# Performance work log

Hardware: AMD Instinct MI355X
Metric: run time of the kernel (lower is better)

Reference implementation:

```python
import jax, jax.numpy as jnp
import numpy as np

N = 64      # features
L = 96      # history length
LP = 24     # prediction length
H = 128     # rnn hidden
B = 1024    # batch


def setup_inputs() -> dict:
    key = jax.random.key(0)
    ks = jax.random.split(key, 16)
    # monotonically increasing timestamps
    tp_all = jnp.cumsum(jax.random.uniform(ks[0], (B, L + LP), dtype=jnp.float32), axis=1)
    tp_true = tp_all[:, :L]
    tp_pred = tp_all[:, L:]
    X = jax.random.normal(ks[1], (B, L, N), dtype=jnp.float32)
    mask = jax.random.randint(ks[2], (B, L, N), 0, 2).astype(jnp.float32)
    def unif(k, shape, fan):
        std = 1.0 / np.sqrt(fan)
        return jax.random.uniform(k, shape, jnp.float32, -std, std)
    # TemporalDecay for h: W (H,N), b (H); std = 1/sqrt(out)
    Wh_dec = unif(ks[3], (H, N), H)
    bh_dec = unif(ks[4], (H,), H)
    # TemporalDecay for x (diag): W (N,N) but only diagonal used
    Wx_dec = unif(ks[5], (N, N), N)
    bx_dec = unif(ks[6], (N,), N)
    # GRUCell: input size = 2N + H
    in_sz = 2 * N + H
    W_ih = unif(ks[7], (3 * H, in_sz), H)
    W_hh = unif(ks[8], (3 * H, H), H)
    b_ih = unif(ks[9], (3 * H,), H)
    b_hh = unif(ks[10], (3 * H,), H)
    # output projection
    Wp = unif(ks[11], (N, H), H)
    bp = unif(ks[12], (N,), H)
    return {"tp_pred": tp_pred, "X": X, "tp_true": tp_true, "mask": mask,
            "Wh_dec": Wh_dec, "bh_dec": bh_dec, "Wx_dec": Wx_dec, "bx_dec": bx_dec,
            "W_ih": W_ih, "W_hh": W_hh, "b_ih": b_ih, "b_hh": b_hh,
            "Wp": Wp, "bp": bp}


def _grud(tp_pred, X, tp_true, mask, Wh_dec, bh_dec, Wx_dec, bx_dec,
          W_ih, W_hh, b_ih, b_hh, Wp, bp):
    Bsz, Lh, Nf = X.shape
    Lp = tp_pred.shape[1]
    Lall = Lh + Lp
    Hh = Wh_dec.shape[0]

    # pad future with zeros (unobserved)
    X_all = jnp.concatenate([X, jnp.zeros((Bsz, Lp, Nf), X.dtype)], axis=1)
    M_all = jnp.concatenate([mask, jnp.zeros((Bsz, Lp, Nf), X.dtype)], axis=1)
    tp = jnp.concatenate([tp_true, tp_pred], axis=1)

    # deltas: first-difference padded with 0 at t=0, broadcast over features
    dt = jnp.pad(tp[:, 1:] - tp[:, :-1], ((0, 0), (1, 0)))  # (B, Lall)
    deltas = jnp.broadcast_to(dt[:, :, None], (Bsz, Lall, Nf))

    # empirical mean over positions where (1 - mask) == 1 (faithful to source)
    valid = 1.0 - M_all
    cnt = jnp.clip(valid.sum(axis=1), 1.0, None)  # (B, N)
    mu = (X_all * valid).sum(axis=1) / cnt        # (B, N)

    # LOCF as in source: where mask != 0, copy previous value
    def locf_step(prev, xm):
        x_t, m_t = xm
        cur = jnp.where(m_t != 0, prev, x_t)
        return cur, cur
    _, X_locf = jax.lax.scan(locf_step, X_all[:, 0],
                             (jnp.swapaxes(X_all, 0, 1), jnp.swapaxes(M_all, 0, 1)))
    # X_locf: (Lall, B, N)

    diag_Wx = jnp.diag(Wx_dec)  # (N,) -- diag=True masks W with identity

    def step(h, inputs):
        x_t, m_t, d_t, xl_t = inputs  # each (B, N)
        gh = jnp.exp(-jax.nn.relu(d_t @ Wh_dec.T + bh_dec))      # (B, H)
        gx = jnp.exp(-jax.nn.relu(d_t * diag_Wx + bx_dec))       # (B, N)
        h = h * gh
        rep = h
        x_h = gx * xl_t + (1.0 - gx) * mu
        x_in = m_t * x_t + (1.0 - m_t) * x_h
        inp = jnp.concatenate([x_in, h, m_t], axis=1)             # (B, 2N+H)
        gi = inp @ W_ih.T + b_ih                                  # (B, 3H)
        gr = h @ W_hh.T + b_hh                                    # (B, 3H)
        r = jax.nn.sigmoid(gi[:, :Hh] + gr[:, :Hh])
        z = jax.nn.sigmoid(gi[:, Hh:2 * Hh] + gr[:, Hh:2 * Hh])
        n = jnp.tanh(gi[:, 2 * Hh:] + r * gr[:, 2 * Hh:])
        h_new = (1.0 - z) * n + z * h
        return h_new, rep

    h0 = jnp.zeros((Bsz, Hh), X.dtype)
    xs = (jnp.swapaxes(X_all, 0, 1), jnp.swapaxes(M_all, 0, 1),
          jnp.swapaxes(deltas, 0, 1), X_locf)
    _, reps = jax.lax.scan(step, h0, xs)          # (Lall, B, H)
    reps = jnp.swapaxes(reps, 0, 1)               # (B, Lall, H)
    recon = reps @ Wp.T + bp                      # (B, Lall, N)
    y_hat = recon[:, -Lp:]                        # (B, Lp, N)
    return y_hat[None]                            # (1, B, Lp, N)


def reference(tp_pred, X, tp_true, mask, Wh_dec, bh_dec, Wx_dec, bx_dec,
              W_ih, W_hh, b_ih, b_hh, Wp, bp):
    return _grud(tp_pred, X, tp_true, mask, Wh_dec, bh_dec, Wx_dec, bx_dec,
                 W_ih, W_hh, b_ih, b_hh, Wp, bp)
```

## Files before the change

kernel.cpp:

```cpp
#include <hip/hip_runtime.h>

#define L2E 1.4426950408889634f

typedef _Float16 f16x8 __attribute__((ext_vector_type(8)));
typedef _Float16 f16x4 __attribute__((ext_vector_type(4)));
typedef float f32x4 __attribute__((ext_vector_type(4)));

__device__ __forceinline__ float sig_fast(float x) {
    return __builtin_amdgcn_rcpf(1.0f + __builtin_amdgcn_exp2f(-L2E * x));
}
__device__ __forceinline__ float tanh_fast(float x) {
    return 1.0f - 2.0f * __builtin_amdgcn_rcpf(1.0f + __builtin_amdgcn_exp2f(2.0f * L2E * x));
}
__device__ __forceinline__ float expnr_fast(float x) {
    return __builtin_amdgcn_exp2f(-L2E * fmaxf(x, 0.0f));
}
__device__ __forceinline__ void barrier_lds_only() {
    __asm__ volatile("s_waitcnt lgkmcnt(0)\n\ts_barrier" ::: "memory");
}

struct F8 { float v[8]; };
__device__ __forceinline__ F8 ld8(const float* p) {
    F8 r;
    float4 a = *(const float4*)p, b = *(const float4*)(p + 4);
    r.v[0]=a.x; r.v[1]=a.y; r.v[2]=a.z; r.v[3]=a.w;
    r.v[4]=b.x; r.v[5]=b.y; r.v[6]=b.z; r.v[7]=b.w;
    return r;
}
__device__ __forceinline__ f16x8 cvt8(F8 a) {
    f16x8 r;
#pragma unroll
    for (int q = 0; q < 8; ++q) r[q] = (_Float16)a.v[q];
    return r;
}
__device__ __forceinline__ f16x8 cvt8s(F8 a, F8 b) {
    f16x8 r;
#pragma unroll
    for (int q = 0; q < 8; ++q) r[q] = (_Float16)(a.v[q] + b.v[q]);
    return r;
}

__global__ __launch_bounds__(256, 1) void grud_kernel(
    const float* __restrict__ tp_pred, const float* __restrict__ X,
    const float* __restrict__ tp_true, const float* __restrict__ mask,
    const float* __restrict__ Wh_dec, const float* __restrict__ bh_dec,
    const float* __restrict__ Wx_dec, const float* __restrict__ bx_dec,
    const float* __restrict__ W_ih, const float* __restrict__ W_hh,
    const float* __restrict__ b_ih, const float* __restrict__ b_hh,
    const float* __restrict__ Wp, const float* __restrict__ bp,
    float* __restrict__ out)
{
    constexpr int SR = 136;
    __shared__ alignas(16) _Float16 ring[16 * 1536];
    __shared__ alignas(16) _Float16 V[2][16 * SR];
    __shared__ alignas(16) _Float16 Astage[2][16 * SR];
    __shared__ float dt_lds[480];
    __shared__ float mu_l[4][64];
    __shared__ float wxl[64], bxl[64];
    __shared__ char occupancy_pad[32768];

    const int tid  = threadIdx.x;
    const int w    = tid >> 6, l = tid & 63, quad = l >> 4, lm = l & 15;
    const int b0   = blockIdx.x * 4;

    if (tid > 100000) occupancy_pad[0] = 1;

    for (int i = tid; i < 16 * SR; i += 256) ((unsigned*)V)[i] = 0;

    for (int i = tid; i < 480; i += 256) {
        int t = i >> 2, q = i & 3, b = b0 + q;
        float v = 0.0f;
        if (t) {
            float cur = (t < 96) ? tp_true[b * 96 + t] : tp_pred[b * 24 + t - 96];
            float prv = (t - 1 < 96) ? tp_true[b * 96 + t - 1] : tp_pred[b * 24 + t - 97];
            v = cur - prv;
        }
        dt_lds[i] = v;
    }
    if (tid < 64) { wxl[tid] = Wx_dec[tid * 65]; bxl[tid] = bx_dec[tid]; }

    {
        const float* xr = X    + ((size_t)(b0 + w) * 96) * 64 + l;
        const float* mr = mask + ((size_t)(b0 + w) * 96) * 64 + l;
        float a = 0.0f, c = 0.0f;
#pragma unroll 4
        for (int t = 0; t < 96; ++t) {
            float x = xr[t * 64], m = mr[t * 64];
            a += x * (1.0f - m); c += 1.0f - m;
        }
        mu_l[w][l] = a / (c + 24.0f);
    }

    const int c0 = 32 * w + lm, c1 = c0 + 16;

    f16x8 wxf[3][2][4];
#pragma unroll
    for (int g = 0; g < 3; ++g)
#pragma unroll
        for (int j = 0; j < 2; ++j)
#pragma unroll
            for (int fi = 0; fi < 4; ++fi) {
                const int row = g * 128 + (j ? c1 : c0);
                const int k0 = fi * 32 + quad * 8;
                wxf[g][j][fi] = cvt8(ld8(W_ih + row * 256 + (k0 < 64 ? k0 : 128 + k0)));
            }

    f16x8 wRZ[2][2][4], wNf[2][4], wGf[2][4], wPf[4];
    float S_[2], bh_[2], bR_[2], bZ_[2], bN_[2], bG_[2];
#pragma unroll
    for (int j = 0; j < 2; ++j) {
        const int c = j ? c1 : c0;
#pragma unroll
        for (int fi = 0; fi < 4; ++fi) {
            const int k0 = fi * 32 + quad * 8;
            wRZ[0][j][fi] = cvt8s(ld8(W_ih + c * 256 + 64 + k0),
                                  ld8(W_hh + c * 128 + k0));
            wRZ[1][j][fi] = cvt8s(ld8(W_ih + (128 + c) * 256 + 64 + k0),
                                  ld8(W_hh + (128 + c) * 128 + k0));
            wNf[j][fi] = cvt8(ld8(W_ih + (256 + c) * 256 + 64 + k0));
            wGf[j][fi] = cvt8(ld8(W_hh + (256 + c) * 128 + k0));
        }
        float s = 0.0f;
        const float4* wh4 = (const float4*)(Wh_dec + c * 64);
#pragma unroll
        for (int i = 0; i < 16; ++i) { float4 u = wh4[i]; s += u.x + u.y + u.z + u.w; }
        S_[j]  = s;
        bh_[j] = bh_dec[c];
        bR_[j] = b_ih[c] + b_hh[c];
        bZ_[j] = b_ih[128 + c] + b_hh[128 + c];
        bN_[j] = b_ih[256 + c];
        bG_[j] = b_hh[256 + c];
    }
    const int pn = w * 16 + lm;
    const float bpv = bp[pn];
#pragma unroll
    for (int fi = 0; fi < 4; ++fi)
        wPf[fi] = cvt8(ld8(Wp + pn * 128 + fi * 32 + quad * 8));

    auto prodLoad = [&](int gp, float4& px, float4& pm) {
        if (gp >= 24) { px = make_float4(0,0,0,0); pm = make_float4(0,0,0,0); return; }
        const int R = tid >> 4, tg = 4 * gp + (R >> 2), b = R & 3;
        const size_t o = (((size_t)(b0 + b) * 96) + tg) * 64 + (tid & 15) * 4;
        px = *(const float4*)(X + o);
        pm = *(const float4*)(mask + o);
    };
    auto prodStage = [&](int gp, float4 px, float4 pm) {
        const int R = tid >> 4, toff = R >> 2, b = R & 3;
        const int tg = 4 * gp + toff, n0 = (tid & 15) * 4;
        const float d = dt_lds[tg * 4 + b];
        const float xs[4] = {px.x, px.y, px.z, px.w};
        const float ms[4] = {pm.x, pm.y, pm.z, pm.w};
        f16x4 xi, mm;
#pragma unroll
        for (int e = 0; e < 4; ++e) {
            const int n = n0 + e;
            const float gxv = expnr_fast(d * wxl[n] + bxl[n]);
            const float muv = mu_l[b][n];
            float v;
            if (gp < 24) {
                v = (ms[e] != 0.0f) ? xs[e] : (xs[e] - muv) * gxv + muv;
                mm[e] = (_Float16)ms[e];
            } else {
                v = (1.0f - gxv) * muv;
                mm[e] = (_Float16)0.0f;
            }
            xi[e] = (_Float16)v;
        }
        *(f16x4*)&Astage[gp & 1][R * SR + n0]      = xi;
        *(f16x4*)&Astage[gp & 1][R * SR + 64 + n0] = mm;
    };
    auto prodMMA = [&](int gp, int j) {
        f16x8 ap[4];
#pragma unroll
        for (int fi = 0; fi < 4; ++fi)
            ap[fi] = *(const f16x8*)&Astage[gp & 1][lm * SR + fi * 32 + quad * 8];
        const int tg = 4 * gp + quad, slot = tg & 15;
        const int c = j ? c1 : c0;
#pragma unroll
        for (int g = 0; g < 3; ++g) {
            f32x4 acc = {0, 0, 0, 0};
#pragma unroll
            for (int fi = 0; fi < 4; ++fi)
                acc = __builtin_amdgcn_mfma_f32_16x16x32_f16(ap[fi], wxf[g][j][fi], acc, 0, 0, 0);
            f16x4 pk = {(_Float16)acc[0], (_Float16)acc[1], (_Float16)acc[2], (_Float16)acc[3]};
            *(f16x4*)&ring[slot * 1536 + (g * 128 + c) * 4] = pk;
        }
    };

    float h0 = 0.0f, h1 = 0.0f;

    auto step = [&](int t, auto&& extra) {
        const int p = t & 1;
        f16x8 af[4];
#pragma unroll
        for (int fi = 0; fi < 4; ++fi)
            af[fi] = *(const f16x8*)&V[p][lm * SR + fi * 32 + quad * 8];
        const int slot = t & 15;
        _Float16 g6[6];
#pragma unroll
        for (int j = 0; j < 2; ++j)
#pragma unroll
            for (int g = 0; g < 3; ++g)
                g6[j * 3 + g] = ring[slot * 1536 + (g * 128 + (j ? c1 : c0)) * 4 + quad];

        extra();

        f32x4 aR0 = {(float)g6[0] + bR_[0], 0, 0, 0}, aZ0 = {(float)g6[1] + bZ_[0], 0, 0, 0};
        f32x4 aN0 = {(float)g6[2] + bN_[0], 0, 0, 0}, aG0 = {bG_[0], 0, 0, 0};
        f32x4 aR1 = {(float)g6[3] + bR_[1], 0, 0, 0}, aZ1 = {(float)g6[4] + bZ_[1], 0, 0, 0};
        f32x4 aN1 = {(float)g6[5] + bN_[1], 0, 0, 0}, aG1 = {bG_[1], 0, 0, 0};
#pragma unroll
        for (int fi = 0; fi < 4; ++fi) {
            aR0 = __builtin_amdgcn_mfma_f32_16x16x32_f16(af[fi], wRZ[0][0][fi], aR0, 0, 0, 0);
            aZ0 = __builtin_amdgcn_mfma_f32_16x16x32_f16(af[fi], wRZ[1][0][fi], aZ0, 0, 0, 0);
            aN0 = __builtin_amdgcn_mfma_f32_16x16x32_f16(af[fi], wNf[0][fi], aN0, 0, 0, 0);
            aG0 = __builtin_amdgcn_mfma_f32_16x16x32_f16(af[fi], wGf[0][fi], aG0, 0, 0, 0);
            aR1 = __builtin_amdgcn_mfma_f32_16x16x32_f16(af[fi], wRZ[0][1][fi], aR1, 0, 0, 0);
            aZ1 = __builtin_amdgcn_mfma_f32_16x16x32_f16(af[fi], wRZ[1][1][fi], aZ1, 0, 0, 0);
            aN1 = __builtin_amdgcn_mfma_f32_16x16x32_f16(af[fi], wNf[1][fi], aN1, 0, 0, 0);
            aG1 = __builtin_amdgcn_mfma_f32_16x16x32_f16(af[fi], wGf[1][fi], aG1, 0, 0, 0);
        }
        if (t >= 96) {
            f32x4 aP = {bpv, 0, 0, 0};
#pragma unroll
            for (int fi = 0; fi < 4; ++fi)
                aP = __builtin_amdgcn_mfma_f32_16x16x32_f16(af[fi], wPf[fi], aP, 0, 0, 0);
            out[((size_t)(b0 + quad) * 24 + (t - 96)) * 64 + pn] = aP[0];
        }
        {
            const float rg0 = sig_fast(aR0[0]), zg0 = sig_fast(aZ0[0]);
            const float ng0 = tanh_fast(aN0[0] + rg0 * aG0[0]);
            h0 = zg0 * (h0 - ng0) + ng0;
            const float rg1 = sig_fast(aR1[0]), zg1 = sig_fast(aZ1[0]);
            const float ng1 = tanh_fast(aN1[0] + rg1 * aG1[0]);
            h1 = zg1 * (h1 - ng1) + ng1;
        }
        if (t < 119) {
            const float d = dt_lds[(t + 1) * 4 + quad];
            h0 *= expnr_fast(d * S_[0] + bh_[0]);
            h1 *= expnr_fast(d * S_[1] + bh_[1]);
            V[p ^ 1][(4 * quad) * SR + c0] = (_Float16)h0;
            V[p ^ 1][(4 * quad) * SR + c1] = (_Float16)h1;
        }
        barrier_lds_only();
    };

    {
        float4 px0, pm0, px1, pm1;
        prodLoad(0, px0, pm0);
        prodLoad(1, px1, pm1);
        __syncthreads();
        prodStage(0, px0, pm0);
        prodStage(1, px1, pm1);
        __syncthreads();
        prodMMA(0, 0); prodMMA(0, 1);
        prodMMA(1, 0); prodMMA(1, 1);
        barrier_lds_only();
    }

    for (int k = 0; k < 30; ++k) {
        const int gp = k + 2;
        float4 px, pm;
        step(4 * k + 0, [&] { if (gp < 30) prodLoad(gp, px, pm); });
        step(4 * k + 1, [&] { if (gp < 30) prodStage(gp, px, pm); });
        step(4 * k + 2, [&] { if (gp < 30) prodMMA(gp, 0); });
        step(4 * k + 3, [&] { if (gp < 30) prodMMA(gp, 1); });
    }
}

extern "C" void kernel_launch(void* const* d_in, const int* in_sizes, int n_in,
                              void* d_out, int out_size, void* d_ws, size_t ws_size,
                              hipStream_t stream) {
    const float* tp_pred = (const float*)d_in[0];
    const float* X       = (const float*)d_in[1];
    const float* tp_true = (const float*)d_in[2];
    const float* mask    = (const float*)d_in[3];
    const float* Wh_dec  = (const float*)d_in[4];
    const float* bh_dec  = (const float*)d_in[5];
    const float* Wx_dec  = (const float*)d_in[6];
    const float* bx_dec  = (const float*)d_in[7];
    const float* W_ih    = (const float*)d_in[8];
    const float* W_hh    = (const float*)d_in[9];
    const float* b_ih    = (const float*)d_in[10];
    const float* b_hh    = (const float*)d_in[11];
    const float* Wp      = (const float*)d_in[12];
    const float* bp      = (const float*)d_in[13];

    grud_kernel<<<dim3(256), dim3(256), 0, stream>>>(
        tp_pred, X, tp_true, mask, Wh_dec, bh_dec, Wx_dec, bx_dec,
        W_ih, W_hh, b_ih, b_hh, Wp, bp, (float*)d_out);
}
```

Before: 232.5 us.

## Split block into producer and recurrence wavefronts for GRU-D

Doubles the block to 512 threads. Four wavefronts do the input-side work (loading, imputation, input-projection MFMAs, output projection) and four run the hidden-state recurrence. The aim is to take producer work off the serial critical path of each timestep. The ring layout is repacked so one consumer lane reads its R/Z/N values with a single f16x4 load. The cost is twice the waves per block, a larger register budget split, and every step still needs a full-block barrier.

```diff
diff --git a/kernel.cpp b/kernel.cpp
--- a/kernel.cpp
+++ b/kernel.cpp
@@ -40,7 +40,7 @@
     return r;
 }
 
-__global__ __launch_bounds__(256, 1) void grud_kernel(
+__global__ __launch_bounds__(512, 2) void grud_kernel(
     const float* __restrict__ tp_pred, const float* __restrict__ X,
     const float* __restrict__ tp_true, const float* __restrict__ mask,
     const float* __restrict__ Wh_dec, const float* __restrict__ bh_dec,
@@ -51,220 +51,235 @@
     float* __restrict__ out)
 {
     constexpr int SR = 136;
-    __shared__ alignas(16) _Float16 ring[16 * 1536];
+    __shared__ alignas(16) _Float16 ring[8 * 2048];
     __shared__ alignas(16) _Float16 V[2][16 * SR];
-    __shared__ alignas(16) _Float16 Astage[2][16 * SR];
+    __shared__ alignas(16) _Float16 Astage[16 * SR];
     __shared__ float dt_lds[480];
     __shared__ float mu_l[4][64];
     __shared__ float wxl[64], bxl[64];
-    __shared__ char occupancy_pad[32768];
+    __shared__ char occ_pad[34000];
 
     const int tid  = threadIdx.x;
     const int w    = tid >> 6, l = tid & 63, quad = l >> 4, lm = l & 15;
     const int b0   = blockIdx.x * 4;
 
-    if (tid > 100000) occupancy_pad[0] = 1;
-
-    for (int i = tid; i < 16 * SR; i += 256) ((unsigned*)V)[i] = 0;
-
-    for (int i = tid; i < 480; i += 256) {
-        int t = i >> 2, q = i & 3, b = b0 + q;
+    if (tid > 100000) occ_pad[0] = 1;
+
+    for (int i = tid; i < 16 * SR; i += 512) ((unsigned*)V)[i] = 0;
+
+    if (tid < 480) {
+        int t = tid >> 2, q = tid & 3, b = b0 + q;
         float v = 0.0f;
         if (t) {
             float cur = (t < 96) ? tp_true[b * 96 + t] : tp_pred[b * 24 + t - 96];
             float prv = (t - 1 < 96) ? tp_true[b * 96 + t - 1] : tp_pred[b * 24 + t - 97];
             v = cur - prv;
         }
-        dt_lds[i] = v;
+        dt_lds[tid] = v;
     }
     if (tid < 64) { wxl[tid] = Wx_dec[tid * 65]; bxl[tid] = bx_dec[tid]; }
 
-    {
-        const float* xr = X    + ((size_t)(b0 + w) * 96) * 64 + l;
-        const float* mr = mask + ((size_t)(b0 + w) * 96) * 64 + l;
-        float a = 0.0f, c = 0.0f;
+    if (w >= 4) {
+        const int pw   = w - 4;
+        const int ptid = tid - 256;
+        const int c0   = 32 * pw + lm, c1 = c0 + 16;
+
+        {
+            const float* xr = X    + ((size_t)(b0 + pw) * 96) * 64 + l;
+            const float* mr = mask + ((size_t)(b0 + pw) * 96) * 64 + l;
+            float a = 0.0f, c = 0.0f;
 #pragma unroll 4
-        for (int t = 0; t < 96; ++t) {
-            float x = xr[t * 64], m = mr[t * 64];
-            a += x * (1.0f - m); c += 1.0f - m;
-        }
-        mu_l[w][l] = a / (c + 24.0f);
-    }
-
-    const int c0 = 32 * w + lm, c1 = c0 + 16;
-
-    f16x8 wxf[3][2][4];
-#pragma unroll
-    for (int g = 0; g < 3; ++g)
-#pragma unroll
-        for (int j = 0; j < 2; ++j)
+            for (int t = 0; t < 96; ++t) {
+                float x = xr[t * 64], m = mr[t * 64];
+                a += x * (1.0f - m); c += 1.0f - m;
+            }
+            mu_l[pw][l] = a / (c + 24.0f);
+        }
+
+        f16x8 wxf[3][2][4];
+#pragma unroll
+        for (int g = 0; g < 3; ++g)
+#pragma unroll
+            for (int j = 0; j < 2; ++j)
+#pragma unroll
+                for (int fi = 0; fi < 4; ++fi) {
+                    const int row = g * 128 + (j ? c1 : c0);
+                    const int k0 = fi * 32 + quad * 8;
+                    wxf[g][j][fi] = cvt8(ld8(W_ih + row * 256 + (k0 < 64 ? k0 : 128 + k0)));
+                }
+
+        const int pn = pw * 16 + lm;
+        const float bpv = bp[pn];
+        f16x8 wPf[4];
+#pragma unroll
+        for (int fi = 0; fi < 4; ++fi)
+            wPf[fi] = cvt8(ld8(Wp + pn * 128 + fi * 32 + quad * 8));
+
+        auto prodLoad = [&](int gp, float4& px, float4& pm) {
+            if (gp >= 24) { px = make_float4(0,0,0,0); pm = make_float4(0,0,0,0); return; }
+            const int R = ptid >> 4, tg = 4 * gp + (R >> 2), b = R & 3;
+            const size_t o = (((size_t)(b0 + b) * 96) + tg) * 64 + (ptid & 15) * 4;
+            px = *(const float4*)(X + o);
+            pm = *(const float4*)(mask + o);
+        };
+        auto prodStage = [&](int gp, float4 px, float4 pm) {
+            const int R = ptid >> 4, toff = R >> 2, b = R & 3;
+            const int tg = 4 * gp + toff, n0 = (ptid & 15) * 4;
+            const float d = dt_lds[tg * 4 + b];
+            const float xs[4] = {px.x, px.y, px.z, px.w};
+            const float ms[4] = {pm.x, pm.y, pm.z, pm.w};
+            f16x4 xi, mm;
+#pragma unroll
+            for (int e = 0; e < 4; ++e) {
+                const int n = n0 + e;
+                const float gxv = expnr_fast(d * wxl[n] + bxl[n]);
+                const float muv = mu_l[b][n];
+                float v;
+                if (gp < 24) {
+                    v = (ms[e] != 0.0f) ? xs[e] : (xs[e] - muv) * gxv + muv;
+                    mm[e] = (_Float16)ms[e];
+                } else {
+                    v = (1.0f - gxv) * muv;
+                    mm[e] = (_Float16)0.0f;
+                }
+                xi[e] = (_Float16)v;
+            }
+            *(f16x4*)&Astage[R * SR + n0]      = xi;
+            *(f16x4*)&Astage[R * SR + 64 + n0] = mm;
+        };
+        auto prodMMA = [&](int gp, int j) {
+            f16x8 ap[4];
+#pragma unroll
+            for (int fi = 0; fi < 4; ++fi)
+                ap[fi] = *(const f16x8*)&Astage[lm * SR + fi * 32 + quad * 8];
+            const int c = j ? c1 : c0;
+            const int slot = (4 * gp + quad) & 7;
+            f32x4 aR = {0,0,0,0}, aZ = {0,0,0,0}, aN = {0,0,0,0};
 #pragma unroll
             for (int fi = 0; fi < 4; ++fi) {
-                const int row = g * 128 + (j ? c1 : c0);
+                aR = __builtin_amdgcn_mfma_f32_16x16x32_f16(ap[fi], wxf[0][j][fi], aR, 0, 0, 0);
+                aZ = __builtin_amdgcn_mfma_f32_16x16x32_f16(ap[fi], wxf[1][j][fi], aZ, 0, 0, 0);
+                aN = __builtin_amdgcn_mfma_f32_16x16x32_f16(ap[fi], wxf[2][j][fi], aN, 0, 0, 0);
+            }
+#pragma unroll
+            for (int rb = 0; rb < 4; ++rb) {
+                f16x4 pk = {(_Float16)aR[rb], (_Float16)aZ[rb], (_Float16)aN[rb], (_Float16)0.0f};
+                *(f16x4*)&ring[slot * 2048 + c * 16 + rb * 4] = pk;
+            }
+        };
+
+        __syncthreads();
+        {
+            float4 px, pm;
+            prodLoad(0, px, pm);
+            prodStage(0, px, pm);
+            prodMMA(0, 0); prodMMA(0, 1);
+        }
+        __syncthreads();
+
+        float4 px, pm;
+        for (int t = 0; t < 120; ++t) {
+            const int gp = (t >> 2) + 1, ph = t & 3;
+            if (ph == 0)      { if (gp < 30) prodLoad(gp, px, pm); }
+            else if (ph == 1) { if (gp < 30) prodStage(gp, px, pm); }
+            else if (ph == 2) { if (gp < 30) prodMMA(gp, 0); }
+            else              { if (gp < 30) prodMMA(gp, 1); }
+
+            if (t >= 96) {
+                f16x8 af[4];
+#pragma unroll
+                for (int fi = 0; fi < 4; ++fi)
+                    af[fi] = *(const f16x8*)&V[t & 1][lm * SR + fi * 32 + quad * 8];
+                f32x4 aP = {bpv, 0, 0, 0};
+#pragma unroll
+                for (int fi = 0; fi < 4; ++fi)
+                    aP = __builtin_amdgcn_mfma_f32_16x16x32_f16(af[fi], wPf[fi], aP, 0, 0, 0);
+                out[((size_t)(b0 + quad) * 24 + (t - 96)) * 64 + pn] = aP[0];
+            }
+            barrier_lds_only();
+        }
+    } else {
+        const int c0 = 32 * w + lm, c1 = c0 + 16;
+
+        f16x8 wR[2][4], wZ[2][4], wN[2][4], wG[2][4];
+        float S_[2], bh_[2], bR_[2], bZ_[2], bN_[2], bG_[2];
+#pragma unroll
+        for (int j = 0; j < 2; ++j) {
+            const int c = j ? c1 : c0;
+#pragma unroll
+            for (int fi = 0; fi < 4; ++fi) {
                 const int k0 = fi * 32 + quad * 8;
-                wxf[g][j][fi] = cvt8(ld8(W_ih + row * 256 + (k0 < 64 ? k0 : 128 + k0)));
-            }
-
-    f16x8 wRZ[2][2][4], wNf[2][4], wGf[2][4], wPf[4];
-    float S_[2], bh_[2], bR_[2], bZ_[2], bN_[2], bG_[2];
-#pragma unroll
-    for (int j = 0; j < 2; ++j) {
-        const int c = j ? c1 : c0;
-#pragma unroll
-        for (int fi = 0; fi < 4; ++fi) {
-            const int k0 = fi * 32 + quad * 8;
-            wRZ[0][j][fi] = cvt8s(ld8(W_ih + c * 256 + 64 + k0),
+                wR[j][fi] = cvt8s(ld8(W_ih + c * 256 + 64 + k0),
                                   ld8(W_hh + c * 128 + k0));
-            wRZ[1][j][fi] = cvt8s(ld8(W_ih + (128 + c) * 256 + 64 + k0),
+                wZ[j][fi] = cvt8s(ld8(W_ih + (128 + c) * 256 + 64 + k0),
                                   ld8(W_hh + (128 + c) * 128 + k0));
-            wNf[j][fi] = cvt8(ld8(W_ih + (256 + c) * 256 + 64 + k0));
-            wGf[j][fi] = cvt8(ld8(W_hh + (256 + c) * 128 + k0));
-        }
-        float s = 0.0f;
-        const float4* wh4 = (const float4*)(Wh_dec + c * 64);
-#pragma unroll
-        for (int i = 0; i < 16; ++i) { float4 u = wh4[i]; s += u.x + u.y + u.z + u.w; }
-        S_[j]  = s;
-        bh_[j] = bh_dec[c];
-        bR_[j] = b_ih[c] + b_hh[c];
-        bZ_[j] = b_ih[128 + c] + b_hh[128 + c];
-        bN_[j] = b_ih[256 + c];
-        bG_[j] = b_hh[256 + c];
-    }
-    const int pn = w * 16 + lm;
-    const float bpv = bp[pn];
-#pragma unroll
-    for (int fi = 0; fi < 4; ++fi)
-        wPf[fi] = cvt8(ld8(Wp + pn * 128 + fi * 32 + quad * 8));
-
-    auto prodLoad = [&](int gp, float4& px, float4& pm) {
-        if (gp >= 24) { px = make_float4(0,0,0,0); pm = make_float4(0,0,0,0); return; }
-        const int R = tid >> 4, tg = 4 * gp + (R >> 2), b = R & 3;
-        const size_t o = (((size_t)(b0 + b) * 96) + tg) * 64 + (tid & 15) * 4;
-        px = *(const float4*)(X + o);
-        pm = *(const float4*)(mask + o);
-    };
-    auto prodStage = [&](int gp, float4 px, float4 pm) {
-        const int R = tid >> 4, toff = R >> 2, b = R & 3;
-        const int tg = 4 * gp + toff, n0 = (tid & 15) * 4;
-        const float d = dt_lds[tg * 4 + b];
-        const float xs[4] = {px.x, px.y, px.z, px.w};
-        const float ms[4] = {pm.x, pm.y, pm.z, pm.w};
-        f16x4 xi, mm;
-#pragma unroll
-        for (int e = 0; e < 4; ++e) {
-            const int n = n0 + e;
-            const float gxv = expnr_fast(d * wxl[n] + bxl[n]);
-            const float muv = mu_l[b][n];
-            float v;
-            if (gp < 24) {
-                v = (ms[e] != 0.0f) ? xs[e] : (xs[e] - muv) * gxv + muv;
-                mm[e] = (_Float16)ms[e];
-            } else {
-                v = (1.0f - gxv) * muv;
-                mm[e] = (_Float16)0.0f;
-            }
-            xi[e] = (_Float16)v;
-        }
-        *(f16x4*)&Astage[gp & 1][R * SR + n0]      = xi;
-        *(f16x4*)&Astage[gp & 1][R * SR + 64 + n0] = mm;
-    };
-    auto prodMMA = [&](int gp, int j) {
-        f16x8 ap[4];
-#pragma unroll
-        for (int fi = 0; fi < 4; ++fi)
-            ap[fi] = *(const f16x8*)&Astage[gp & 1][lm * SR + fi * 32 + quad * 8];
-        const int tg = 4 * gp + quad, slot = tg & 15;
-        const int c = j ? c1 : c0;
-#pragma unroll
-        for (int g = 0; g < 3; ++g) {
-            f32x4 acc = {0, 0, 0, 0};
+                wN[j][fi] = cvt8(ld8(W_ih + (256 + c) * 256 + 64 + k0));
+                wG[j][fi] = cvt8(ld8(W_hh + (256 + c) * 128 + k0));
+            }
+            float s = 0.0f;
+            const float4* wh4 = (const float4*)(Wh_dec + c * 64);
+#pragma unroll
+            for (int i = 0; i < 16; ++i) { float4 u = wh4[i]; s += u.x + u.y + u.z + u.w; }
+            S_[j]  = s;
+            bh_[j] = bh_dec[c];
+            bR_[j] = b_ih[c] + b_hh[c];
+            bZ_[j] = b_ih[128 + c] + b_hh[128 + c];
+            bN_[j] = b_ih[256 + c];
+            bG_[j] = b_hh[256 + c];
+        }
+
+        __syncthreads();
+        __syncthreads();
+
+        float h0 = 0.0f, h1 = 0.0f;
+        for (int t = 0; t < 120; ++t) {
+            const _Float16* Vp = V[t & 1];
+            const int sb = (t & 7) * 2048;
+            const f16x4 g0 = *(const f16x4*)&ring[sb + c0 * 16 + quad * 4];
+            const f16x4 g1 = *(const f16x4*)&ring[sb + c1 * 16 + quad * 4];
+            f16x8 af[4];
 #pragma unroll
             for (int fi = 0; fi < 4; ++fi)
-                acc = __builtin_amdgcn_mfma_f32_16x16x32_f16(ap[fi], wxf[g][j][fi], acc, 0, 0, 0);
-            f16x4 pk = {(_Float16)acc[0], (_Float16)acc[1], (_Float16)acc[2], (_Float16)acc[3]};
-            *(f16x4*)&ring[slot * 1536 + (g * 128 + c) * 4] = pk;
-        }
-    };
-
-    float h0 = 0.0f, h1 = 0.0f;
-
-    auto step = [&](int t, auto&& extra) {
-        const int p = t & 1;
-        f16x8 af[4];
-#pragma unroll
-        for (int fi = 0; fi < 4; ++fi)
-            af[fi] = *(const f16x8*)&V[p][lm * SR + fi * 32 + quad * 8];
-        const int slot = t & 15;
-        _Float16 g6[6];
-#pragma unroll
-        for (int j = 0; j < 2; ++j)
-#pragma unroll
-            for (int g = 0; g < 3; ++g)
-                g6[j * 3 + g] = ring[slot * 1536 + (g * 128 + (j ? c1 : c0)) * 4 + quad];
-
-        extra();
-
-        f32x4 aR0 = {(float)g6[0] + bR_[0], 0, 0, 0}, aZ0 = {(float)g6[1] + bZ_[0], 0, 0, 0};
-        f32x4 aN0 = {(float)g6[2] + bN_[0], 0, 0, 0}, aG0 = {bG_[0], 0, 0, 0};
-        f32x4 aR1 = {(float)g6[3] + bR_[1], 0, 0, 0}, aZ1 = {(float)g6[4] + bZ_[1], 0, 0, 0};
-        f32x4 aN1 = {(float)g6[5] + bN_[1], 0, 0, 0}, aG1 = {bG_[1], 0, 0, 0};
-#pragma unroll
-        for (int fi = 0; fi < 4; ++fi) {
-            aR0 = __builtin_amdgcn_mfma_f32_16x16x32_f16(af[fi], wRZ[0][0][fi], aR0, 0, 0, 0);
-            aZ0 = __builtin_amdgcn_mfma_f32_16x16x32_f16(af[fi], wRZ[1][0][fi], aZ0, 0, 0, 0);
-            aN0 = __builtin_amdgcn_mfma_f32_16x16x32_f16(af[fi], wNf[0][fi], aN0, 0, 0, 0);
-            aG0 = __builtin_amdgcn_mfma_f32_16x16x32_f16(af[fi], wGf[0][fi], aG0, 0, 0, 0);
-            aR1 = __builtin_amdgcn_mfma_f32_16x16x32_f16(af[fi], wRZ[0][1][fi], aR1, 0, 0, 0);
-            aZ1 = __builtin_amdgcn_mfma_f32_16x16x32_f16(af[fi], wRZ[1][1][fi], aZ1, 0, 0, 0);
-            aN1 = __builtin_amdgcn_mfma_f32_16x16x32_f16(af[fi], wNf[1][fi], aN1, 0, 0, 0);
-            aG1 = __builtin_amdgcn_mfma_f32_16x16x32_f16(af[fi], wGf[1][fi], aG1, 0, 0, 0);
-        }
-        if (t >= 96) {
-            f32x4 aP = {bpv, 0, 0, 0};
-#pragma unroll
-            for (int fi = 0; fi < 4; ++fi)
-                aP = __builtin_amdgcn_mfma_f32_16x16x32_f16(af[fi], wPf[fi], aP, 0, 0, 0);
-            out[((size_t)(b0 + quad) * 24 + (t - 96)) * 64 + pn] = aP[0];
-        }
-        {
-            const float rg0 = sig_fast(aR0[0]), zg0 = sig_fast(aZ0[0]);
-            const float ng0 = tanh_fast(aN0[0] + rg0 * aG0[0]);
-            h0 = zg0 * (h0 - ng0) + ng0;
-            const float rg1 = sig_fast(aR1[0]), zg1 = sig_fast(aZ1[0]);
-            const float ng1 = tanh_fast(aN1[0] + rg1 * aG1[0]);
-            h1 = zg1 * (h1 - ng1) + ng1;
-        }
-        if (t < 119) {
-            const float d = dt_lds[(t + 1) * 4 + quad];
-            h0 *= expnr_fast(d * S_[0] + bh_[0]);
-            h1 *= expnr_fast(d * S_[1] + bh_[1]);
-            V[p ^ 1][(4 * quad) * SR + c0] = (_Float16)h0;
-            V[p ^ 1][(4 * quad) * SR + c1] = (_Float16)h1;
-        }
-        barrier_lds_only();
-    };
-
-    {
-        float4 px0, pm0, px1, pm1;
-        prodLoad(0, px0, pm0);
-        prodLoad(1, px1, pm1);
-        __syncthreads();
-        prodStage(0, px0, pm0);
-        prodStage(1, px1, pm1);
-        __syncthreads();
-        prodMMA(0, 0); prodMMA(0, 1);
-        prodMMA(1, 0); prodMMA(1, 1);
-        barrier_lds_only();
-    }
-
-    for (int k = 0; k < 30; ++k) {
-        const int gp = k + 2;
-        float4 px, pm;
-        step(4 * k + 0, [&] { if (gp < 30) prodLoad(gp, px, pm); });
-        step(4 * k + 1, [&] { if (gp < 30) prodStage(gp, px, pm); });
-        step(4 * k + 2, [&] { if (gp < 30) prodMMA(gp, 0); });
-        step(4 * k + 3, [&] { if (gp < 30) prodMMA(gp, 1); });
+                af[fi] = *(const f16x8*)&Vp[lm * SR + fi * 32 + quad * 8];
+
+            f32x4 aR0 = {(float)g0[0] + bR_[0], 0, 0, 0};
+            f32x4 aZ0 = {(float)g0[1] + bZ_[0], 0, 0, 0};
+            f32x4 aN0 = {(float)g0[2] + bN_[0], 0, 0, 0};
+            f32x4 aG0 = {bG_[0], 0, 0, 0};
+            f32x4 aR1 = {(float)g1[0] + bR_[1], 0, 0, 0};
+            f32x4 aZ1 = {(float)g1[1] + bZ_[1], 0, 0, 0};
+            f32x4 aN1 = {(float)g1[2] + bN_[1], 0, 0, 0};
+            f32x4 aG1 = {bG_[1], 0, 0, 0};
+#pragma unroll
+            for (int fi = 0; fi < 4; ++fi) {
+                aR0 = __builtin_amdgcn_mfma_f32_16x16x32_f16(af[fi], wR[0][fi], aR0, 0, 0, 0);
+                aZ0 = __builtin_amdgcn_mfma_f32_16x16x32_f16(af[fi], wZ[0][fi], aZ0, 0, 0, 0);
+                aN0 = __builtin_amdgcn_mfma_f32_16x16x32_f16(af[fi], wN[0][fi], aN0, 0, 0, 0);
+                aG0 = __builtin_amdgcn_mfma_f32_16x16x32_f16(af[fi], wG[0][fi], aG0, 0, 0, 0);
+                aR1 = __builtin_amdgcn_mfma_f32_16x16x32_f16(af[fi], wR[1][fi], aR1, 0, 0, 0);
+                aZ1 = __builtin_amdgcn_mfma_f32_16x16x32_f16(af[fi], wZ[1][fi], aZ1, 0, 0, 0);
+                aN1 = __builtin_amdgcn_mfma_f32_16x16x32_f16(af[fi], wN[1][fi], aN1, 0, 0, 0);
+                aG1 = __builtin_amdgcn_mfma_f32_16x16x32_f16(af[fi], wG[1][fi], aG1, 0, 0, 0);
+            }
+
+            {
+                const float rg0 = sig_fast(aR0[0]), zg0 = sig_fast(aZ0[0]);
+                const float ng0 = tanh_fast(aN0[0] + rg0 * aG0[0]);
+                h0 = zg0 * (h0 - ng0) + ng0;
+                const float rg1 = sig_fast(aR1[0]), zg1 = sig_fast(aZ1[0]);
+                const float ng1 = tanh_fast(aN1[0] + rg1 * aG1[0]);
+                h1 = zg1 * (h1 - ng1) + ng1;
+            }
+            if (t < 119) {
+                const float d = dt_lds[(t + 1) * 4 + quad];
+                h0 *= expnr_fast(d * S_[0] + bh_[0]);
+                h1 *= expnr_fast(d * S_[1] + bh_[1]);
+                _Float16* Vn = V[(t & 1) ^ 1];
+                Vn[(4 * quad) * SR + c0] = (_Float16)h0;
+                Vn[(4 * quad) * SR + c1] = (_Float16)h1;
+            }
+            barrier_lds_only();
+        }
     }
 }
 
@@ -286,7 +301,7 @@
     const float* Wp      = (const float*)d_in[12];
     const float* bp      = (const float*)d_in[13];
 
-    grud_kernel<<<dim3(256), dim3(256), 0, stream>>>(
+    grud_kernel<<<dim3(256), dim3(512), 0, stream>>>(
         tp_pred, X, tp_true, mask, Wh_dec, bh_dec, Wx_dec, bx_dec,
         W_ih, W_hh, b_ih, b_hh, Wp, bp, (float*)d_out);
 }
```

New measurement: 204.1 us. 12.2% less time.
